# Kernel tuning notes

Measured on AMD Instinct MI355X. Metric: run time of the kernel, lower is better.

The kernel has to match this reference:

```python
import jax, jax.numpy as jnp
import numpy as np

GBT_ALPHA = 0.5


def _hippo_legs(N):
    # HiPPO-LegS transition: A[n,k] = -sqrt(2n+1)sqrt(2k+1) (n>k), -(n+1) (n==k); B[n]=sqrt(2n+1)
    n = jnp.arange(N, dtype=jnp.float32)
    q = jnp.sqrt(2.0 * n + 1.0)
    A = -jnp.where(n[:, None] > n[None, :], q[:, None] * q[None, :], 0.0) - jnp.diag(n + 1.0)
    B = q
    return A, B


def setup_inputs() -> dict:
    key = jax.random.key(0)
    k1, k2 = jax.random.split(key, 2)
    T, Bsz, N, O = 1024, 512, 256, 10
    inputs = jax.random.normal(k1, (T, Bsz, 1), dtype=jnp.float32)
    mlp_w = jax.random.normal(k2, (O, N), dtype=jnp.float32) / np.float32(np.sqrt(N))
    mlp_b = jnp.zeros((O,), dtype=jnp.float32)
    return {"inputs": inputs, "mlp_w": mlp_w, "mlp_b": mlp_b}


def reference(inputs, mlp_w, mlp_b):
    # inputs: [T, B, 1]; HiPPO-LegS recurrence with GBT(alpha) discretization, dt_t = 1/(t+1)
    T, Bsz, _ = inputs.shape
    N = mlp_w.shape[1]
    A, Bv = _hippo_legs(N)
    I = jnp.eye(N, dtype=inputs.dtype)
    dts = 1.0 / jnp.arange(1, T + 1, dtype=inputs.dtype)  # [T]

    def disc(dt):
        lhs = I - dt * GBT_ALPHA * A
        Ad = jnp.linalg.solve(lhs, I + dt * (1.0 - GBT_ALPHA) * A)  # [N,N]
        Bd = dt * jnp.linalg.solve(lhs, Bv)                         # [N]
        return Ad, Bd

    Ads, Bds = jax.vmap(disc)(dts)  # [T,N,N], [T,N]

    def step(c, xs):
        Ad, Bd, f = xs                       # Ad [N,N], Bd [N], f [B,1]
        c = c @ Ad.T + f * Bd[None, :]       # [B,N]
        return c, None

    c0 = jnp.zeros((Bsz, N), dtype=inputs.dtype)
    cT, _ = jax.lax.scan(step, c0, (Ads, Bds, inputs))
    # MLP head (single linear N -> output_size)
    return cT @ mlp_w.T + mlp_b
```

## Files before the change

kernel.cpp:

```cpp
#include <hip/hip_runtime.h>
#include <math.h>

#define T_STEPS 1024
#define BSZ     512
#define NDIM    256
#define ODIM    10
#define NCH     8
#define CT      128
#define NCHUNK  8
#define CHUNK   128

template<int CTRL, int RMASK>
__device__ __forceinline__ float dpp_fetch(float x, float ident) {
    return __int_as_float(__builtin_amdgcn_update_dpp(
        __float_as_int(ident), __float_as_int(x), CTRL, RMASK, 0xF, false));
}

#define SCAN_ROUND(CTRL, RMASK)                                   \
    {   const float Ap = dpp_fetch<CTRL, RMASK>(Ac, 1.0f);        \
        const float Bp = dpp_fetch<CTRL, RMASK>(Bc, 0.0f);        \
        Bc = fmaf(Ac, Bp, Bc);                                    \
        Ac = Ac * Ap; }

#define SCAN2(CTRL, RMASK)                                        \
    {   const float Ap  = dpp_fetch<CTRL, RMASK>(Ac,  1.0f);      \
        const float Bp0 = dpp_fetch<CTRL, RMASK>(Bc0, 0.0f);      \
        const float Bp1 = dpp_fetch<CTRL, RMASK>(Bc1, 0.0f);      \
        Bc0 = fmaf(Ac, Bp0, Bc0);                                 \
        Bc1 = fmaf(Ac, Bp1, Bc1);                                 \
        Ac  = Ac * Ap; }

__device__ __forceinline__ float fast_rcp(float x) {
    float r = __builtin_amdgcn_rcpf(x);
    return fmaf(r, fmaf(-x, r, 1.0f), r);
}

__device__ __forceinline__ void init_kmaps(int lane, float kp1[4], float tk2[4]) {
#pragma unroll
    for (int j = 0; j < 4; ++j) {
        const int k = 255 - (4 * lane + j);
        kp1[j] = (float)(k + 1);
        tk2[j] = (float)(2 * (2 * k + 1));
    }
}

__global__ __launch_bounds__(64, 1) void chunk_kernel(float* __restrict__ PT,
                                                      float* __restrict__ WcT) {
    const int bx   = blockIdx.x;
    const int c    = blockIdx.y;
    const int lane = threadIdx.x;
    const int i0   = 2 * bx;

    float kp1[4], tk2[4], G0[4], G1[4];
    init_kmaps(lane, kp1, tk2);
#pragma unroll
    for (int j = 0; j < 4; ++j) {
        const int k = 255 - (4 * lane + j);
        G0[j] = (k == i0)     ? 1.0f : 0.0f;
        G1[j] = (k == i0 + 1) ? 1.0f : 0.0f;
    }

    float* wrow = WcT + (size_t)c * CT * NDIM + i0;
    const int tend = (c + 1) * CT, tstart = c * CT;
    float tf = (float)tend;
    for (int t = tend; t > tstart; --t) {
        const float dt = fast_rcp(tf);
        const float a  = 0.5f * dt;

        float e[4], al[4], rr[4], be0[4], be1[4];
#pragma unroll
        for (int j = 0; j < 4; ++j) {
            const float denom = fmaf(a, kp1[j], 1.0f);
            const float d     = fast_rcp(denom);
            const float ad    = a * d;
            e[j]   = fmaf(2.0f, d, -1.0f);
            al[j]  = e[j] + ad;
            rr[j]  = ad * tk2[j];
            be0[j] = d * G0[j];
            be1[j] = d * G1[j];
        }

        float Ac = al[0], Bc0 = be0[0], Bc1 = be1[0];
#pragma unroll
        for (int j = 1; j < 4; ++j) {
            Bc0 = fmaf(al[j], Bc0, be0[j]);
            Bc1 = fmaf(al[j], Bc1, be1[j]);
            Ac *= al[j];
        }

        SCAN2(0x111, 0xF)
        SCAN2(0x112, 0xF)
        SCAN2(0x114, 0xF)
        SCAN2(0x118, 0xF)
        SCAN2(0x142, 0xA)
        {
            const float Bp0 = dpp_fetch<0x143, 0xC>(Bc0, 0.0f);
            const float Bp1 = dpp_fetch<0x143, 0xC>(Bc1, 0.0f);
            Bc0 = fmaf(Ac, Bp0, Bc0);
            Bc1 = fmaf(Ac, Bp1, Bc1);
        }

        float S0 = dpp_fetch<0x138, 0xF>(Bc0, 0.0f);
        float S1 = dpp_fetch<0x138, 0xF>(Bc1, 0.0f);
#pragma unroll
        for (int j = 0; j < 4; ++j) {
            G0[j] = fmaf(-rr[j], S0, e[j] * G0[j]);
            G1[j] = fmaf(-rr[j], S1, e[j] * G1[j]);
            S0 = fmaf(al[j], S0, be0[j]);
            S1 = fmaf(al[j], S1, be1[j]);
        }

        if (lane == 63)
            *(float2*)(wrow + (size_t)(t - tstart - 1) * NDIM) =
                make_float2(dt * S0, dt * S1);
        tf -= 1.0f;
    }

#pragma unroll
    for (int j = 0; j < 4; ++j) {
        const int k = 255 - (4 * lane + j);
        *(float2*)(PT + ((size_t)c * NDIM + k) * NDIM + i0) =
            make_float2(G0[j], G1[j]);
    }
}

__global__ __launch_bounds__(256) void r_kernel(const float* __restrict__ mlp_w,
                                                const float* __restrict__ PT,
                                                float* __restrict__ R) {
    const int o   = blockIdx.x;
    const int tid = threadIdx.x;

    __shared__ float Gs[NDIM];
    Gs[tid] = sqrtf(2.0f * (float)tid + 1.0f) * mlp_w[o * NDIM + tid];
    __syncthreads();

    for (int c = NCH - 1; c >= 0; --c) {
        R[((size_t)c * ODIM + o) * NDIM + tid] = Gs[tid];
        if (c > 0) {
            const float4* row = (const float4*)(PT + ((size_t)c * NDIM + tid) * NDIM);
            float a0 = 0.f, a1 = 0.f, a2 = 0.f, a3 = 0.f;
#pragma unroll 8
            for (int ii = 0; ii < NDIM / 4; ++ii) {
                const float4 r4 = row[ii];
                a0 = fmaf(r4.x, Gs[4 * ii + 0], a0);
                a1 = fmaf(r4.y, Gs[4 * ii + 1], a1);
                a2 = fmaf(r4.z, Gs[4 * ii + 2], a2);
                a3 = fmaf(r4.w, Gs[4 * ii + 3], a3);
            }
            const float y = (a0 + a1) + (a2 + a3);
            __syncthreads();
            Gs[tid] = y;
            __syncthreads();
        }
    }
}

__global__ __launch_bounds__(256) void z_kernel(const float* __restrict__ WcT,
                                                const float* __restrict__ R,
                                                float* __restrict__ weff) {
    __shared__ float Rl[ODIM * NDIM];
    const int tid = threadIdx.x;
    const int r0  = blockIdx.x * 4;
    const int c   = r0 / CT;

    for (int idx = tid; idx < ODIM * NDIM; idx += 256)
        Rl[idx] = R[(size_t)c * ODIM * NDIM + idx];
    __syncthreads();

    const int w    = tid >> 6;
    const int lane = tid & 63;
    const int r    = r0 + w;
    const float4 w4 = *(const float4*)(WcT + (size_t)r * NDIM + 4 * lane);

#pragma unroll
    for (int o = 0; o < ODIM; ++o) {
        const float* Ro = Rl + o * NDIM + 4 * lane;
        float p = fmaf(w4.x, Ro[0], fmaf(w4.y, Ro[1],
                  fmaf(w4.z, Ro[2], w4.w * Ro[3])));
#pragma unroll
        for (int m = 1; m < 64; m <<= 1) p += __shfl_xor(p, m);
        if (lane == o) weff[(size_t)r * ODIM + o] = p;
    }
}

__device__ __forceinline__ float wstep(float G[4], const float kp1[4],
                                       const float tk2[4], float tf) {
    const float dt = fast_rcp(tf);
    const float a  = 0.5f * dt;

    float e[4], al[4], rr[4], be[4];
#pragma unroll
    for (int j = 0; j < 4; ++j) {
        const float denom = fmaf(a, kp1[j], 1.0f);
        const float d     = fast_rcp(denom);
        const float ad    = a * d;
        e[j]  = fmaf(2.0f, d, -1.0f);
        al[j] = e[j] + ad;
        rr[j] = ad * tk2[j];
        be[j] = d * G[j];
    }

    float Ac = al[0], Bc = be[0];
#pragma unroll
    for (int j = 1; j < 4; ++j) { Bc = fmaf(al[j], Bc, be[j]); Ac *= al[j]; }

    SCAN_ROUND(0x111, 0xF)
    SCAN_ROUND(0x112, 0xF)
    SCAN_ROUND(0x114, 0xF)
    SCAN_ROUND(0x118, 0xF)
    SCAN_ROUND(0x142, 0xA)
    {
        const float Bp = dpp_fetch<0x143, 0xC>(Bc, 0.0f);
        Bc = fmaf(Ac, Bp, Bc);
    }

    float S = dpp_fetch<0x138, 0xF>(Bc, 0.0f);
#pragma unroll
    for (int j = 0; j < 4; ++j) {
        G[j] = fmaf(-rr[j], S, e[j] * G[j]);
        S    = fmaf(al[j], S, be[j]);
    }
    return dt * S;
}

__global__ __launch_bounds__(64) void weff_kernel(const float* __restrict__ mlp_w,
                                                  float* __restrict__ weff) {
    const int o    = blockIdx.x;
    const int lane = threadIdx.x;

    float kp1[4], tk2[4], G[4];
    init_kmaps(lane, kp1, tk2);
#pragma unroll
    for (int j = 0; j < 4; ++j) {
        const int k = 255 - (4 * lane + j);
        G[j] = sqrtf((float)(2 * k + 1)) * mlp_w[o * NDIM + k];
    }

    float tf = (float)T_STEPS;
#pragma unroll 2
    for (int t = T_STEPS; t >= 1; --t) {
        const float w = wstep(G, kp1, tk2, tf);
        if (lane == 63) weff[(t - 1) * ODIM + o] = w;
        tf -= 1.0f;
    }
}

__global__ __launch_bounds__(128) void partial_kernel(const float* __restrict__ f,
                                                      const float* __restrict__ weff,
                                                      float* __restrict__ part) {
    __shared__ float wsm[CHUNK * ODIM];
    const int tid = threadIdx.x;
    const int b   = blockIdx.x * 128 + tid;
    const int tc  = blockIdx.y;
    const int t0  = tc * CHUNK;

    for (int i = tid; i < CHUNK * ODIM; i += 128)
        wsm[i] = weff[t0 * ODIM + i];
    __syncthreads();

    float acc[ODIM];
#pragma unroll
    for (int o = 0; o < ODIM; ++o) acc[o] = 0.0f;

    for (int tt = 0; tt < CHUNK; ++tt) {
        const float fv = f[(t0 + tt) * BSZ + b];
#pragma unroll
        for (int o = 0; o < ODIM; ++o)
            acc[o] = fmaf(fv, wsm[tt * ODIM + o], acc[o]);
    }

#pragma unroll
    for (int o = 0; o < ODIM; ++o)
        part[(tc * BSZ + b) * ODIM + o] = acc[o];
}

__global__ __launch_bounds__(256) void reduce_kernel(const float* __restrict__ part,
                                                     const float* __restrict__ mlp_b,
                                                     float* __restrict__ out) {
    const int i = blockIdx.x * 256 + threadIdx.x;
    if (i >= BSZ * ODIM) return;
    const int o = i % ODIM;
    float s = mlp_b[o];
#pragma unroll
    for (int c = 0; c < NCHUNK; ++c) s += part[c * BSZ * ODIM + i];
    out[i] = s;
}

extern "C" void kernel_launch(void* const* d_in, const int* in_sizes, int n_in,
                              void* d_out, int out_size, void* d_ws, size_t ws_size,
                              hipStream_t stream) {
    const float* inputs = (const float*)d_in[0];
    const float* mlp_w  = (const float*)d_in[1];
    const float* mlp_b  = (const float*)d_in[2];
    float* out = (float*)d_out;

    const size_t PT_elems   = (size_t)NCH * NDIM * NDIM;
    const size_t WcT_elems  = (size_t)NCH * CT * NDIM;
    const size_t R_elems    = (size_t)NCH * ODIM * NDIM;
    const size_t weff_elems = (size_t)T_STEPS * ODIM;
    const size_t part_elems = (size_t)NCHUNK * BSZ * ODIM;
    const size_t need = (PT_elems + WcT_elems + R_elems + weff_elems + part_elems)
                        * sizeof(float);

    if (ws_size >= need) {
        float* PT   = (float*)d_ws;
        float* WcT  = PT + PT_elems;
        float* R    = WcT + WcT_elems;
        float* weff = R + R_elems;
        float* part = weff + weff_elems;
        chunk_kernel<<<dim3(NDIM / 2, NCH), 64, 0, stream>>>(PT, WcT);
        r_kernel<<<ODIM, NDIM, 0, stream>>>(mlp_w, PT, R);
        z_kernel<<<T_STEPS / 4, 256, 0, stream>>>(WcT, R, weff);
        partial_kernel<<<dim3(BSZ / 128, NCHUNK), 128, 0, stream>>>(inputs, weff, part);
        reduce_kernel<<<(BSZ * ODIM + 255) / 256, 256, 0, stream>>>(part, mlp_b, out);
    } else {
        float* weff = (float*)d_ws;
        float* part = weff + weff_elems;
        weff_kernel<<<ODIM, 64, 0, stream>>>(mlp_w, weff);
        partial_kernel<<<dim3(BSZ / 128, NCHUNK), 128, 0, stream>>>(inputs, weff, part);
        reduce_kernel<<<(BSZ * ODIM + 255) / 256, 256, 0, stream>>>(part, mlp_b, out);
    }
}
```

Baseline: 198.5 us.

## Split time into more chunks, widen per-wave columns, parallelize r_kernel reduction

The time axis is now split into 16 chunks instead of 8, which halves the serial length of each chunk_kernel wave. Each wave now carries 4 columns (V=4) instead of 2, so more work is amortized per DPP scan. r_kernel moves from 256 to 1024 threads, with four threads per row and a reduction through shared memory. The chain of dependent r_kernel steps doubles, partial_kernel uses 32 smaller chunks, and a fallback path for 8 chunks is kept for smaller workspaces.

```diff
diff --git a/kernel.cpp b/kernel.cpp
--- a/kernel.cpp
+++ b/kernel.cpp
@@ -5,10 +5,8 @@
 #define BSZ     512
 #define NDIM    256
 #define ODIM    10
-#define NCH     8
-#define CT      128
-#define NCHUNK  8
-#define CHUNK   128
+#define NCHUNK  32
+#define CHUNK   32
 
 template<int CTRL, int RMASK>
 __device__ __forceinline__ float dpp_fetch(float x, float ident) {
@@ -22,13 +20,14 @@
         Bc = fmaf(Ac, Bp, Bc);                                    \
         Ac = Ac * Ap; }
 
-#define SCAN2(CTRL, RMASK)                                        \
-    {   const float Ap  = dpp_fetch<CTRL, RMASK>(Ac,  1.0f);      \
-        const float Bp0 = dpp_fetch<CTRL, RMASK>(Bc0, 0.0f);      \
-        const float Bp1 = dpp_fetch<CTRL, RMASK>(Bc1, 0.0f);      \
-        Bc0 = fmaf(Ac, Bp0, Bc0);                                 \
-        Bc1 = fmaf(Ac, Bp1, Bc1);                                 \
-        Ac  = Ac * Ap; }
+#define SCANV(CTRL, RMASK)                                        \
+    {   const float Ap = dpp_fetch<CTRL, RMASK>(Ac, 1.0f);        \
+        _Pragma("unroll")                                         \
+        for (int v = 0; v < V; ++v) {                             \
+            const float Bp = dpp_fetch<CTRL, RMASK>(Bc[v], 0.0f); \
+            Bc[v] = fmaf(Ac, Bp, Bc[v]);                          \
+        }                                                         \
+        Ac = Ac * Ap; }
 
 __device__ __forceinline__ float fast_rcp(float x) {
     float r = __builtin_amdgcn_rcpf(x);
@@ -44,117 +43,147 @@
     }
 }
 
-__global__ __launch_bounds__(64, 1) void chunk_kernel(float* __restrict__ PT,
-                                                      float* __restrict__ WcT) {
-    const int bx   = blockIdx.x;
+template<int NCH, int V>
+__global__ __launch_bounds__(64) void chunk_kernel(float* __restrict__ PT,
+                                                   float* __restrict__ WcT) {
+    constexpr int CT = T_STEPS / NCH;
+    const int g    = blockIdx.x;
     const int c    = blockIdx.y;
     const int lane = threadIdx.x;
-    const int i0   = 2 * bx;
-
-    float kp1[4], tk2[4], G0[4], G1[4];
+    const int i0   = V * g;
+
+    float kp1[4], tk2[4];
     init_kmaps(lane, kp1, tk2);
-#pragma unroll
-    for (int j = 0; j < 4; ++j) {
-        const int k = 255 - (4 * lane + j);
-        G0[j] = (k == i0)     ? 1.0f : 0.0f;
-        G1[j] = (k == i0 + 1) ? 1.0f : 0.0f;
-    }
+    float G[V][4];
+#pragma unroll
+    for (int v = 0; v < V; ++v)
+#pragma unroll
+        for (int j = 0; j < 4; ++j) {
+            const int k = 255 - (4 * lane + j);
+            G[v][j] = (k == i0 + v) ? 1.0f : 0.0f;
+        }
 
     float* wrow = WcT + (size_t)c * CT * NDIM + i0;
     const int tend = (c + 1) * CT, tstart = c * CT;
     float tf = (float)tend;
+#pragma unroll 2
     for (int t = tend; t > tstart; --t) {
         const float dt = fast_rcp(tf);
         const float a  = 0.5f * dt;
 
-        float e[4], al[4], rr[4], be0[4], be1[4];
+        float e[4], al[4], rr[4], be[V][4];
 #pragma unroll
         for (int j = 0; j < 4; ++j) {
             const float denom = fmaf(a, kp1[j], 1.0f);
             const float d     = fast_rcp(denom);
             const float ad    = a * d;
-            e[j]   = fmaf(2.0f, d, -1.0f);
-            al[j]  = e[j] + ad;
-            rr[j]  = ad * tk2[j];
-            be0[j] = d * G0[j];
-            be1[j] = d * G1[j];
-        }
-
-        float Ac = al[0], Bc0 = be0[0], Bc1 = be1[0];
+            e[j]  = fmaf(2.0f, d, -1.0f);
+            al[j] = e[j] + ad;
+            rr[j] = ad * tk2[j];
+#pragma unroll
+            for (int v = 0; v < V; ++v) be[v][j] = d * G[v][j];
+        }
+
+        float Ac = al[0];
+        float Bc[V];
+#pragma unroll
+        for (int v = 0; v < V; ++v) Bc[v] = be[v][0];
 #pragma unroll
         for (int j = 1; j < 4; ++j) {
-            Bc0 = fmaf(al[j], Bc0, be0[j]);
-            Bc1 = fmaf(al[j], Bc1, be1[j]);
+#pragma unroll
+            for (int v = 0; v < V; ++v) Bc[v] = fmaf(al[j], Bc[v], be[v][j]);
             Ac *= al[j];
         }
 
-        SCAN2(0x111, 0xF)
-        SCAN2(0x112, 0xF)
-        SCAN2(0x114, 0xF)
-        SCAN2(0x118, 0xF)
-        SCAN2(0x142, 0xA)
+        SCANV(0x111, 0xF)
+        SCANV(0x112, 0xF)
+        SCANV(0x114, 0xF)
+        SCANV(0x118, 0xF)
+        SCANV(0x142, 0xA)
         {
-            const float Bp0 = dpp_fetch<0x143, 0xC>(Bc0, 0.0f);
-            const float Bp1 = dpp_fetch<0x143, 0xC>(Bc1, 0.0f);
-            Bc0 = fmaf(Ac, Bp0, Bc0);
-            Bc1 = fmaf(Ac, Bp1, Bc1);
-        }
-
-        float S0 = dpp_fetch<0x138, 0xF>(Bc0, 0.0f);
-        float S1 = dpp_fetch<0x138, 0xF>(Bc1, 0.0f);
+#pragma unroll
+            for (int v = 0; v < V; ++v) {
+                const float Bp = dpp_fetch<0x143, 0xC>(Bc[v], 0.0f);
+                Bc[v] = fmaf(Ac, Bp, Bc[v]);
+            }
+        }
+
+        float S[V];
+#pragma unroll
+        for (int v = 0; v < V; ++v)
+            S[v] = dpp_fetch<0x138, 0xF>(Bc[v], 0.0f);
+
 #pragma unroll
         for (int j = 0; j < 4; ++j) {
-            G0[j] = fmaf(-rr[j], S0, e[j] * G0[j]);
-            G1[j] = fmaf(-rr[j], S1, e[j] * G1[j]);
-            S0 = fmaf(al[j], S0, be0[j]);
-            S1 = fmaf(al[j], S1, be1[j]);
-        }
-
-        if (lane == 63)
-            *(float2*)(wrow + (size_t)(t - tstart - 1) * NDIM) =
-                make_float2(dt * S0, dt * S1);
+#pragma unroll
+            for (int v = 0; v < V; ++v) {
+                G[v][j] = fmaf(-rr[j], S[v], e[j] * G[v][j]);
+                S[v]    = fmaf(al[j], S[v], be[v][j]);
+            }
+        }
+
+        if (lane == 63) {
+            float* wp = wrow + (size_t)(t - tstart - 1) * NDIM;
+            if constexpr (V == 4)
+                *(float4*)wp = make_float4(dt * S[0], dt * S[1], dt * S[2], dt * S[3]);
+            else
+                *(float2*)wp = make_float2(dt * S[0], dt * S[1]);
+        }
         tf -= 1.0f;
     }
 
 #pragma unroll
     for (int j = 0; j < 4; ++j) {
         const int k = 255 - (4 * lane + j);
-        *(float2*)(PT + ((size_t)c * NDIM + k) * NDIM + i0) =
-            make_float2(G0[j], G1[j]);
-    }
-}
-
-__global__ __launch_bounds__(256) void r_kernel(const float* __restrict__ mlp_w,
-                                                const float* __restrict__ PT,
-                                                float* __restrict__ R) {
+        float* pp = PT + ((size_t)c * NDIM + k) * NDIM + i0;
+        if constexpr (V == 4)
+            *(float4*)pp = make_float4(G[0][j], G[1][j], G[2][j], G[3][j]);
+        else
+            *(float2*)pp = make_float2(G[0][j], G[1][j]);
+    }
+}
+
+template<int NCH>
+__global__ __launch_bounds__(1024) void r_kernel(const float* __restrict__ mlp_w,
+                                                 const float* __restrict__ PT,
+                                                 float* __restrict__ R) {
     const int o   = blockIdx.x;
     const int tid = threadIdx.x;
+    const int k   = tid >> 2;
+    const int q   = tid & 3;
 
     __shared__ float Gs[NDIM];
-    Gs[tid] = sqrtf(2.0f * (float)tid + 1.0f) * mlp_w[o * NDIM + tid];
+    __shared__ float red[1024];
+    if (tid < NDIM)
+        Gs[tid] = sqrtf(2.0f * (float)tid + 1.0f) * mlp_w[o * NDIM + tid];
     __syncthreads();
 
     for (int c = NCH - 1; c >= 0; --c) {
-        R[((size_t)c * ODIM + o) * NDIM + tid] = Gs[tid];
+        if (tid < NDIM) R[((size_t)c * ODIM + o) * NDIM + tid] = Gs[tid];
         if (c > 0) {
-            const float4* row = (const float4*)(PT + ((size_t)c * NDIM + tid) * NDIM);
+            const float4* row =
+                (const float4*)(PT + ((size_t)c * NDIM + k) * NDIM + q * 64);
+            const float* gq = Gs + q * 64;
             float a0 = 0.f, a1 = 0.f, a2 = 0.f, a3 = 0.f;
-#pragma unroll 8
-            for (int ii = 0; ii < NDIM / 4; ++ii) {
+#pragma unroll
+            for (int ii = 0; ii < 16; ++ii) {
                 const float4 r4 = row[ii];
-                a0 = fmaf(r4.x, Gs[4 * ii + 0], a0);
-                a1 = fmaf(r4.y, Gs[4 * ii + 1], a1);
-                a2 = fmaf(r4.z, Gs[4 * ii + 2], a2);
-                a3 = fmaf(r4.w, Gs[4 * ii + 3], a3);
+                a0 = fmaf(r4.x, gq[4 * ii + 0], a0);
+                a1 = fmaf(r4.y, gq[4 * ii + 1], a1);
+                a2 = fmaf(r4.z, gq[4 * ii + 2], a2);
+                a3 = fmaf(r4.w, gq[4 * ii + 3], a3);
             }
-            const float y = (a0 + a1) + (a2 + a3);
+            red[tid] = (a0 + a1) + (a2 + a3);
             __syncthreads();
-            Gs[tid] = y;
+            if (tid < NDIM)
+                Gs[tid] = (red[4 * tid] + red[4 * tid + 1]) +
+                          (red[4 * tid + 2] + red[4 * tid + 3]);
             __syncthreads();
         }
     }
 }
 
+template<int CT>
 __global__ __launch_bounds__(256) void z_kernel(const float* __restrict__ WcT,
                                                 const float* __restrict__ R,
                                                 float* __restrict__ weff) {
@@ -262,6 +291,7 @@
 #pragma unroll
     for (int o = 0; o < ODIM; ++o) acc[o] = 0.0f;
 
+#pragma unroll 4
     for (int tt = 0; tt < CHUNK; ++tt) {
         const float fv = f[(t0 + tt) * BSZ + b];
 #pragma unroll
@@ -294,23 +324,37 @@
     const float* mlp_b  = (const float*)d_in[2];
     float* out = (float*)d_out;
 
-    const size_t PT_elems   = (size_t)NCH * NDIM * NDIM;
-    const size_t WcT_elems  = (size_t)NCH * CT * NDIM;
-    const size_t R_elems    = (size_t)NCH * ODIM * NDIM;
+    const size_t WcT_elems  = (size_t)T_STEPS * NDIM;
     const size_t weff_elems = (size_t)T_STEPS * ODIM;
     const size_t part_elems = (size_t)NCHUNK * BSZ * ODIM;
-    const size_t need = (PT_elems + WcT_elems + R_elems + weff_elems + part_elems)
-                        * sizeof(float);
-
-    if (ws_size >= need) {
+
+    auto need = [&](int nch) {
+        return ((size_t)nch * NDIM * NDIM + WcT_elems +
+                (size_t)nch * ODIM * NDIM + weff_elems + part_elems) * sizeof(float);
+    };
+
+    if (ws_size >= need(16)) {
+        constexpr int NCH = 16, V = 4, CT = T_STEPS / NCH;
         float* PT   = (float*)d_ws;
-        float* WcT  = PT + PT_elems;
+        float* WcT  = PT + (size_t)NCH * NDIM * NDIM;
         float* R    = WcT + WcT_elems;
-        float* weff = R + R_elems;
+        float* weff = R + (size_t)NCH * ODIM * NDIM;
         float* part = weff + weff_elems;
-        chunk_kernel<<<dim3(NDIM / 2, NCH), 64, 0, stream>>>(PT, WcT);
-        r_kernel<<<ODIM, NDIM, 0, stream>>>(mlp_w, PT, R);
-        z_kernel<<<T_STEPS / 4, 256, 0, stream>>>(WcT, R, weff);
+        chunk_kernel<NCH, V><<<dim3(NDIM / V, NCH), 64, 0, stream>>>(PT, WcT);
+        r_kernel<NCH><<<ODIM, 1024, 0, stream>>>(mlp_w, PT, R);
+        z_kernel<CT><<<T_STEPS / 4, 256, 0, stream>>>(WcT, R, weff);
+        partial_kernel<<<dim3(BSZ / 128, NCHUNK), 128, 0, stream>>>(inputs, weff, part);
+        reduce_kernel<<<(BSZ * ODIM + 255) / 256, 256, 0, stream>>>(part, mlp_b, out);
+    } else if (ws_size >= need(8)) {
+        constexpr int NCH = 8, V = 2, CT = T_STEPS / NCH;
+        float* PT   = (float*)d_ws;
+        float* WcT  = PT + (size_t)NCH * NDIM * NDIM;
+        float* R    = WcT + WcT_elems;
+        float* weff = R + (size_t)NCH * ODIM * NDIM;
+        float* part = weff + weff_elems;
+        chunk_kernel<NCH, V><<<dim3(NDIM / V, NCH), 64, 0, stream>>>(PT, WcT);
+        r_kernel<NCH><<<ODIM, 1024, 0, stream>>>(mlp_w, PT, R);
+        z_kernel<CT><<<T_STEPS / 4, 256, 0, stream>>>(WcT, R, weff);
         partial_kernel<<<dim3(BSZ / 128, NCHUNK), 128, 0, stream>>>(inputs, weff, part);
         reduce_kernel<<<(BSZ * ODIM + 255) / 256, 256, 0, stream>>>(part, mlp_b, out);
     } else {
```

New measurement: 271.8 us. 36.9% more time.
